# Kernel optimization log

Hardware: AMD Instinct MI355X
Metric: run time of the kernel (lower is better)

## Reference

```python
import math
import jax, jax.numpy as jnp
import numpy as np

D, NH, NL, NP = 256, 8, 4, 4
C = D // NH
VALUE_SHAPES = np.array([[128, 128], [64, 64], [32, 32], [16, 16]], dtype=np.int32)


def _offset_bias():
    # Faithful to MSDeformAttn._reset_parameters grid init for sampling_offsets.bias
    th = np.arange(NH, dtype=np.float32) * (2.0 * np.pi / NH)
    g = np.stack([np.cos(th), np.sin(th)], -1)                      # [NH,2]
    g = g / np.abs(g).max(-1, keepdims=True)
    g = np.tile(g[:, None, None, :], (1, NL, NP, 1))                # [NH,NL,NP,2]
    g = g * np.arange(1, NP + 1, dtype=np.float32)[None, None, :, None]
    return jnp.asarray(g.reshape(-1), jnp.float32)


def setup_inputs() -> dict:
    key = jax.random.key(0)
    ks = jax.random.split(key, 10)
    bs, Q = 8, 2048
    LV = int((VALUE_SHAPES[:, 0] * VALUE_SHAPES[:, 1]).sum())
    s = 0.02
    return {
        "query": jax.random.normal(ks[0], (bs, Q, D), jnp.float32),
        "refer_bbox": jax.random.uniform(ks[1], (bs, Q, NL, 2), jnp.float32),
        "value": jax.random.normal(ks[2], (bs, LV, D), jnp.float32),
        "value_shapes": VALUE_SHAPES,  # static numpy (shapes must be compile-time constants)
        "W_value": jax.random.normal(ks[3], (D, D), jnp.float32) * s,
        "b_value": jnp.zeros((D,), jnp.float32),
        "W_off": jax.random.normal(ks[4], (D, NH * NL * NP * 2), jnp.float32) * 0.01,
        "b_off": _offset_bias(),
        "W_attn": jax.random.normal(ks[5], (D, NH * NL * NP), jnp.float32) * s,
        "b_attn": jnp.zeros((NH * NL * NP,), jnp.float32),
        "W_out": jax.random.normal(ks[6], (D, D), jnp.float32) * s,
        "b_out": jnp.zeros((D,), jnp.float32),
    }


def _ms_deform_attn(value, shapes, loc, attn):
    # value: [bs,LV,NH,C], loc: [bs,Q,NH,NL,NP,2] in [0,1], attn: [bs,Q,NH,NL,NP]
    bs, LV = value.shape[:2]
    Q = loc.shape[1]
    BH = bs * NH
    v = value.transpose(0, 2, 1, 3).reshape(BH, LV, C)              # [BH,LV,C]
    loc = loc.transpose(0, 2, 1, 3, 4, 5).reshape(BH, Q, NL, NP, 2)
    attn = attn.transpose(0, 2, 1, 3, 4).reshape(BH, Q, NL, NP)
    acc = jnp.zeros((BH, Q, C), value.dtype)
    start = 0
    for lvl in range(NL):
        H, W = int(shapes[lvl, 0]), int(shapes[lvl, 1])
        img = v[:, start:start + H * W]                             # [BH,HW,C]
        start += H * W
        # grid_sample(align_corners=False): pixel coord = loc * size - 0.5
        x = loc[:, :, lvl, :, 0] * W - 0.5                          # [BH,Q,NP]
        y = loc[:, :, lvl, :, 1] * H - 0.5
        x0 = jnp.floor(x); y0 = jnp.floor(y)
        fx = x - x0; fy = y - y0
        x0i = x0.astype(jnp.int32); y0i = y0.astype(jnp.int32)
        samp = jnp.zeros((BH, Q, NP, C), value.dtype)
        for dx, dy in ((0, 0), (1, 0), (0, 1), (1, 1)):
            xi = x0i + dx; yi = y0i + dy
            valid = (xi >= 0) & (xi < W) & (yi >= 0) & (yi < H)     # zero padding
            w = (fx if dx else 1.0 - fx) * (fy if dy else 1.0 - fy)
            w = jnp.where(valid, w, 0.0)
            idx = jnp.clip(yi, 0, H - 1) * W + jnp.clip(xi, 0, W - 1)
            g = jnp.take_along_axis(img, idx.reshape(BH, Q * NP)[..., None], axis=1)
            samp = samp + w[..., None] * g.reshape(BH, Q, NP, C)
        acc = acc + (samp * attn[:, :, lvl, :, None]).sum(2)
    return acc.reshape(bs, NH, Q, C).transpose(0, 2, 1, 3).reshape(bs, Q, D)


def reference(query, refer_bbox, value, value_shapes, W_value, b_value,
              W_off, b_off, W_attn, b_attn, W_out, b_out):
    shapes = np.asarray(value_shapes)  # static
    bs, Q = query.shape[:2]
    LV = value.shape[1]
    v = (value @ W_value + b_value).reshape(bs, LV, NH, C)
    off = (query @ W_off + b_off).reshape(bs, Q, NH, NL, NP, 2)
    attn = jax.nn.softmax((query @ W_attn + b_attn).reshape(bs, Q, NH, NL * NP), -1)
    attn = attn.reshape(bs, Q, NH, NL, NP)
    norm = jnp.asarray(shapes[:, ::-1], query.dtype)                # (W,H) per level
    loc = refer_bbox[:, :, None, :, None, :] + off / norm[None, None, None, :, None, :]
    out = _ms_deform_attn(v, shapes, loc, attn)
    return out @ W_out + b_out
```

## Files before the change

kernel.cpp:

```cpp
#include <hip/hip_runtime.h>
#include <hip/hip_bf16.h>

#define D_MODEL 256
#define NHEAD   8
#define NLVL    4
#define NPTS    4
#define CH      32
#define QTOT    2048
#define BS      8
#define LVTOT   21760
#define KDIM    256

typedef __attribute__((ext_vector_type(8))) short bf16x8;
typedef __attribute__((ext_vector_type(4))) float f32x4;

__device__ inline float bf_lo(unsigned u) { unsigned t = u << 16; float f; __builtin_memcpy(&f, &t, 4); return f; }
__device__ inline float bf_hi(unsigned u) { unsigned t = u & 0xffff0000u; float f; __builtin_memcpy(&f, &t, 4); return f; }
__device__ inline float bfu2f(unsigned short s) { unsigned t = (unsigned)s << 16; float f; __builtin_memcpy(&f, &t, 4); return f; }
__device__ inline unsigned short f2bfu(float f) { __hip_bfloat16 h = __float2bfloat16(f); unsigned short u; __builtin_memcpy(&u, &h, 2); return u; }

#define BK  64
#define LDP 72
#define LDC2 136

__device__ inline void transpose_W_body(const float* __restrict__ W,
                                        __hip_bfloat16* __restrict__ Wt,
                                        int sh, int blk, int tid) {
    int t = blk * 256 + tid;
    int k = t >> sh, n = t & ((1 << sh) - 1);
    Wt[n * 256 + k] = __float2bfloat16(W[(k << sh) + n]);
}

__global__ __launch_bounds__(256)
void convert_all(const float* __restrict__ q, __hip_bfloat16* __restrict__ qb,
                 const float* __restrict__ Wv, __hip_bfloat16* __restrict__ Wtv,
                 const float* __restrict__ Wo, __hip_bfloat16* __restrict__ Wto,
                 const float* __restrict__ Wa, __hip_bfloat16* __restrict__ Wta) {
    const int bid = blockIdx.x;
    const int tid = threadIdx.x;
    if (bid < 4096) {
        int t = bid * 256 + tid;
        float4 f = ((const float4*)q)[t];
        __hip_bfloat16 h4[4] = {__float2bfloat16(f.x), __float2bfloat16(f.y),
                                __float2bfloat16(f.z), __float2bfloat16(f.w)};
        ((uint2*)qb)[t] = *(const uint2*)h4;
    } else if (bid < 4352) {
        transpose_W_body(Wv, Wtv, 8, bid - 4096, tid);
    } else if (bid < 4608) {
        transpose_W_body(Wo, Wto, 8, bid - 4352, tid);
    } else {
        transpose_W_body(Wa, Wta, 7, bid - 4608, tid);
    }
}

__global__ __launch_bounds__(256)
void convert_W(const float* __restrict__ W, __hip_bfloat16* __restrict__ Wt, int sh) {
    int t = blockIdx.x * 256 + threadIdx.x;
    int k = t >> sh, n = t & ((1 << sh) - 1);
    Wt[n * 256 + k] = __float2bfloat16(W[(k << sh) + n]);
}

__device__ void value_gemm_body(char* smem, int bid_v,
                                const float* __restrict__ A,
                                const __hip_bfloat16* __restrict__ Wt,
                                const float* __restrict__ bias,
                                __hip_bfloat16* __restrict__ v) {
    __hip_bfloat16* As = (__hip_bfloat16*)smem;
    __hip_bfloat16* Bs = (__hip_bfloat16*)(smem + 128 * LDP * 2);
    __hip_bfloat16* Cs = (__hip_bfloat16*)smem;

    const int tid  = threadIdx.x;
    const int lane = tid & 63;
    const int wave = tid >> 6;
    const int wr   = wave >> 1;
    const int wc   = wave & 1;
    const int cb      = (bid_v & 1) * 128;
    const int rowBase = (bid_v >> 1) * 128;

    const int m0   = lane & 15;
    const int quad = lane >> 4;

    const int ar = tid >> 4;
    const int ac = tid & 15;
    const int br = tid >> 3;
    const int bc = tid & 7;

    f32x4 acc[4][4] = {};

    for (int kc = 0; kc < KDIM; kc += BK) {
#pragma unroll
        for (int i = 0; i < 8; ++i) {
            const int row = i * 16 + ar;
            float4 f = *(const float4*)(A + (size_t)(rowBase + row) * KDIM + kc + ac * 4);
            __hip_bfloat16 t4[4] = {__float2bfloat16(f.x), __float2bfloat16(f.y),
                                    __float2bfloat16(f.z), __float2bfloat16(f.w)};
            *(uint2*)&As[row * LDP + ac * 4] = *(const uint2*)t4;
        }
#pragma unroll
        for (int i = 0; i < 4; ++i) {
            const int row = i * 32 + br;
            uint4 u = *(const uint4*)(Wt + (size_t)(cb + row) * KDIM + kc + bc * 8);
            *(uint4*)&Bs[row * LDP + bc * 8] = u;
        }
        __syncthreads();

#pragma unroll
        for (int ks = 0; ks < 2; ++ks) {
            bf16x8 af[4], bfv[4];
#pragma unroll
            for (int i = 0; i < 4; ++i)
                af[i] = *(const bf16x8*)&As[(wr * 64 + i * 16 + m0) * LDP + ks * 32 + quad * 8];
#pragma unroll
            for (int j = 0; j < 4; ++j)
                bfv[j] = *(const bf16x8*)&Bs[(wc * 64 + j * 16 + m0) * LDP + ks * 32 + quad * 8];
#pragma unroll
            for (int i = 0; i < 4; ++i)
#pragma unroll
                for (int j = 0; j < 4; ++j)
                    acc[i][j] = __builtin_amdgcn_mfma_f32_16x16x32_bf16(af[i], bfv[j], acc[i][j], 0, 0, 0);
        }
        __syncthreads();
    }

    const int b = rowBase / LVTOT;
    const int pixBase = rowBase - b * LVTOT;
#pragma unroll
    for (int half = 0; half < 2; ++half) {
        if (wr == half) {
#pragma unroll
            for (int j = 0; j < 4; ++j) {
                const int lcol = wc * 64 + j * 16 + m0;
                const float bv = bias[cb + lcol];
#pragma unroll
                for (int i = 0; i < 4; ++i) {
                    const int lrow = i * 16 + quad * 4;
#pragma unroll
                    for (int r = 0; r < 4; ++r)
                        Cs[(lrow + r) * LDC2 + lcol] = __float2bfloat16(acc[i][j][r] + bv);
                }
            }
        }
        __syncthreads();
        char* dst = (char*)v + (size_t)(b * LVTOT + pixBase + half * 64) * 512 + cb * 2;
        const char* src = (const char*)Cs;
#pragma unroll
        for (int itr = 0; itr < 4; ++itr) {
            const int o = itr * 4096 + tid * 16;
            const int row = o >> 8;
            const int c   = o & 255;
            uint4 val = *(const uint4*)(src + row * (LDC2 * 2) + c);
            *(uint4*)(dst + (size_t)row * 512 + c) = val;
        }
        if (half == 0) __syncthreads();
    }
}

__device__ void offattn_gemm_body(char* smem, int bid,
                                  const __hip_bfloat16* __restrict__ A,
                                  const __hip_bfloat16* __restrict__ Wt_oa,
                                  const float* __restrict__ b_off,
                                  const float* __restrict__ b_attn,
                                  float* __restrict__ off_ws,
                                  float* __restrict__ logits_ws) {
    __hip_bfloat16* As = (__hip_bfloat16*)smem;
    __hip_bfloat16* Bs = (__hip_bfloat16*)(smem + 128 * LDP * 2);

    const int tid  = threadIdx.x;
    const int lane = tid & 63;
    const int wave = tid >> 6;
    const int rowBase = (bid & 127) * 128;
    const int cb      = (bid >> 7) * 128;

    const int m0   = lane & 15;
    const int quad = lane >> 4;

    const int br = tid >> 3;
    const int bc = tid & 7;

    f32x4 acc[2][8] = {};

    for (int kc = 0; kc < KDIM; kc += BK) {
#pragma unroll
        for (int i = 0; i < 4; ++i) {
            const int row = i * 32 + br;
            uint4 ua = *(const uint4*)(A     + (size_t)(rowBase + row) * KDIM + kc + bc * 8);
            uint4 ub = *(const uint4*)(Wt_oa + (size_t)(cb + row) * KDIM + kc + bc * 8);
            *(uint4*)&As[row * LDP + bc * 8] = ua;
            *(uint4*)&Bs[row * LDP + bc * 8] = ub;
        }
        __syncthreads();

#pragma unroll
        for (int ks = 0; ks < 2; ++ks) {
            bf16x8 af[2], bfv[8];
#pragma unroll
            for (int i = 0; i < 2; ++i)
                af[i] = *(const bf16x8*)&As[(wave * 32 + i * 16 + m0) * LDP + ks * 32 + quad * 8];
#pragma unroll
            for (int j = 0; j < 8; ++j)
                bfv[j] = *(const bf16x8*)&Bs[(j * 16 + m0) * LDP + ks * 32 + quad * 8];
#pragma unroll
            for (int i = 0; i < 2; ++i)
#pragma unroll
                for (int j = 0; j < 8; ++j)
                    acc[i][j] = __builtin_amdgcn_mfma_f32_16x16x32_bf16(af[i], bfv[j], acc[i][j], 0, 0, 0);
        }
        __syncthreads();
    }

#pragma unroll
    for (int j = 0; j < 8; ++j) {
        const int col = cb + j * 16 + m0;
        const bool isOff = (col < 256);
        const float bv = isOff ? b_off[col] : b_attn[col - 256];
#pragma unroll
        for (int i = 0; i < 2; ++i) {
            const int row0 = rowBase + wave * 32 + i * 16 + quad * 4;
#pragma unroll
            for (int r = 0; r < 4; ++r) {
                const float val = acc[i][j][r] + bv;
                if (isOff) off_ws[(size_t)(row0 + r) * 256 + col] = val;
                else       logits_ws[(size_t)(row0 + r) * 128 + (col - 256)] = val;
            }
        }
    }
}

__global__ __launch_bounds__(256, 2)
void fused_gemms(const float* __restrict__ value,
                 const __hip_bfloat16* __restrict__ Wt_v,
                 const float* __restrict__ b_value,
                 __hip_bfloat16* __restrict__ v_ws,
                 const __hip_bfloat16* __restrict__ q_bf,
                 const __hip_bfloat16* __restrict__ Wt_oa,
                 const float* __restrict__ b_off,
                 const float* __restrict__ b_attn,
                 float* __restrict__ off_ws,
                 float* __restrict__ logits_ws) {
    __shared__ __align__(16) char smem[36864];
    const int bid = blockIdx.x;
    if (bid < 384) {
        offattn_gemm_body(smem, bid, q_bf, Wt_oa, b_off, b_attn, off_ws, logits_ws);
    } else {
        value_gemm_body(smem, bid - 384, value, Wt_v, b_value, v_ws);
    }
}

struct StorePlain {
    float* o;
    int ncol;
    __device__ void operator()(int row, int col, float val) const {
        o[(size_t)row * ncol + col] = val;
    }
};

template <typename Store>
__global__ __launch_bounds__(256, 2)
void gemm_bf16_mfma(const __hip_bfloat16* __restrict__ A,
                    const __hip_bfloat16* __restrict__ Wt,
                    const float* __restrict__ bias, Store store) {
    __shared__ __align__(16) __hip_bfloat16 As[128 * LDP];
    __shared__ __align__(16) __hip_bfloat16 Bs[128 * LDP];

    const int tid  = threadIdx.x;
    const int lane = tid & 63;
    const int wave = tid >> 6;
    const int rowBase = blockIdx.x * 128;
    const int cb = blockIdx.y * 128;

    const int m0   = lane & 15;
    const int quad = lane >> 4;

    const int br = tid >> 3;
    const int bc = tid & 7;

    f32x4 acc[2][8] = {};

    for (int kc = 0; kc < KDIM; kc += BK) {
#pragma unroll
        for (int i = 0; i < 4; ++i) {
            const int row = i * 32 + br;
            uint4 ua = *(const uint4*)(A  + (size_t)(rowBase + row) * KDIM + kc + bc * 8);
            uint4 ub = *(const uint4*)(Wt + (size_t)(cb + row) * KDIM + kc + bc * 8);
            *(uint4*)&As[row * LDP + bc * 8] = ua;
            *(uint4*)&Bs[row * LDP + bc * 8] = ub;
        }
        __syncthreads();

#pragma unroll
        for (int ks = 0; ks < 2; ++ks) {
            bf16x8 af[2], bfv[8];
#pragma unroll
            for (int i = 0; i < 2; ++i)
                af[i] = *(const bf16x8*)&As[(wave * 32 + i * 16 + m0) * LDP + ks * 32 + quad * 8];
#pragma unroll
            for (int j = 0; j < 8; ++j)
                bfv[j] = *(const bf16x8*)&Bs[(j * 16 + m0) * LDP + ks * 32 + quad * 8];
#pragma unroll
            for (int i = 0; i < 2; ++i)
#pragma unroll
                for (int j = 0; j < 8; ++j)
                    acc[i][j] = __builtin_amdgcn_mfma_f32_16x16x32_bf16(af[i], bfv[j], acc[i][j], 0, 0, 0);
        }
        __syncthreads();
    }

#pragma unroll
    for (int j = 0; j < 8; ++j) {
        const int col = cb + j * 16 + m0;
        const float bv = bias[col];
#pragma unroll
        for (int i = 0; i < 2; ++i) {
            const int row0 = rowBase + wave * 32 + i * 16 + quad * 4;
#pragma unroll
            for (int r = 0; r < 4; ++r)
                store(row0 + r, col, acc[i][j][r] + bv);
        }
    }
}

__global__ __launch_bounds__(256, 5)
void sample_kernel(const float* __restrict__ off_ws,
                   const float* __restrict__ logits_ws,
                   const float* __restrict__ bbox,
                   const __hip_bfloat16* __restrict__ v,
                   __hip_bfloat16* __restrict__ acc_bf) {
    __shared__ __align__(16) float off_s[8 * 256];
    __shared__ __align__(16) float attn_s[8 * 128];
    __shared__ float bbox_s[64];
    __shared__ __align__(8) unsigned short idx_s[1024 * 4];
    __shared__ __align__(8) unsigned short w_s[1024 * 4];

    const int tid = threadIdx.x;
    const int b = blockIdx.x & 7;
    const int gq0 = b * QTOT + (blockIdx.x >> 3) * 8;

    const float4* osrc = (const float4*)(off_ws + (size_t)gq0 * 256);
    ((float4*)off_s)[tid] = osrc[tid];
    ((float4*)off_s)[tid + 256] = osrc[tid + 256];
    const float4* lsrc = (const float4*)(logits_ws + (size_t)gq0 * 128);
    ((float4*)attn_s)[tid] = lsrc[tid];
    if (tid < 64) bbox_s[tid] = bbox[(size_t)gq0 * 8 + tid];
    __syncthreads();

    if (tid < 64) {
        int qq = tid >> 3, h = tid & 7;
        float* p = attn_s + qq * 128 + h * 16;
        float m = p[0];
#pragma unroll
        for (int i = 1; i < 16; ++i) m = fmaxf(m, p[i]);
        float e[16], s = 0.f;
#pragma unroll
        for (int i = 0; i < 16; ++i) { e[i] = __expf(p[i] - m); s += e[i]; }
        float inv = 1.f / s;
#pragma unroll
        for (int i = 0; i < 16; ++i) p[i] = e[i] * inv;
    }
    __syncthreads();

#pragma unroll
    for (int r = 0; r < 4; ++r) {
        const int tap = tid + r * 256;
        const int qq = tap >> 7, h = (tap >> 4) & 7, l = (tap >> 2) & 3, p = tap & 3;
        const int Wd = 128 >> l;
        const int st = (l == 0) ? 0 : (l == 1) ? 16384 : (l == 2) ? 20480 : 21504;

        const float bx = bbox_s[qq * 8 + l * 2 + 0];
        const float by = bbox_s[qq * 8 + l * 2 + 1];
        const float ox = off_s[qq * 256 + h * 32 + l * 8 + p * 2 + 0];
        const float oy = off_s[qq * 256 + h * 32 + l * 8 + p * 2 + 1];
        const float att = attn_s[qq * 128 + h * 16 + l * 4 + p];

        const float x = bx * (float)Wd + ox - 0.5f;
        const float y = by * (float)Wd + oy - 0.5f;
        const float x0f = floorf(x), y0f = floorf(y);
        const float fx = x - x0f, fy = y - y0f;
        const int x0 = (int)x0f, y0 = (int)y0f;
        const int x1 = x0 + 1, y1 = y0 + 1;
        const bool vx0 = (unsigned)x0 < (unsigned)Wd;
        const bool vx1 = (unsigned)x1 < (unsigned)Wd;
        const bool vy0 = (unsigned)y0 < (unsigned)Wd;
        const bool vy1 = (unsigned)y1 < (unsigned)Wd;
        const int cx0 = min(max(x0, 0), Wd - 1), cx1 = min(max(x1, 0), Wd - 1);
        const int cy0 = min(max(y0, 0), Wd - 1), cy1 = min(max(y1, 0), Wd - 1);

        unsigned short pi[4];
        pi[0] = (unsigned short)(st + cy0 * Wd + cx0);
        pi[1] = (unsigned short)(st + cy0 * Wd + cx1);
        pi[2] = (unsigned short)(st + cy1 * Wd + cx0);
        pi[3] = (unsigned short)(st + cy1 * Wd + cx1);
        float w0 = (vx0 && vy0) ? (1.f - fx) * (1.f - fy) * att : 0.f;
        float w1 = (vx1 && vy0) ? fx * (1.f - fy) * att : 0.f;
        float w2 = (vx0 && vy1) ? (1.f - fx) * fy * att : 0.f;
        float w3 = (vx1 && vy1) ? fx * fy * att : 0.f;

        *(uint2*)&idx_s[tap * 4] = *(const uint2*)pi;
        unsigned short w4[4] = {f2bfu(w0), f2bfu(w1), f2bfu(w2), f2bfu(w3)};
        *(uint2*)&w_s[tap * 4] = *(const uint2*)w4;
    }
    __syncthreads();

    const int lane = tid & 63;
    const int wave = tid >> 6;
    const int g  = lane >> 3;
    const int c4 = lane & 7;

    const char* vbase = (const char*)v + (size_t)b * LVTOT * 512 + c4 * 8;

    for (int i = 0; i < 8; ++i) {
        const int pairA = wave * 16 + 2 * i;
        const int pairB = pairA + 1;
        const int qqA = pairA >> 3, hhA = pairA & 7;
        const int qqB = pairB >> 3, hhB = pairB & 7;
        const char* slabA = vbase + hhA * 64;
        const char* slabB = vbase + hhB * 64;
        const int tbA = qqA * 128 + hhA * 16;
        const int tbB = qqB * 128 + hhB * 16;

        const ushort4 pA0 = *(const ushort4*)&idx_s[(tbA + g) * 4];
        const ushort4 pA1 = *(const ushort4*)&idx_s[(tbA + 8 + g) * 4];
        const ushort4 pB0 = *(const ushort4*)&idx_s[(tbB + g) * 4];
        const ushort4 pB1 = *(const ushort4*)&idx_s[(tbB + 8 + g) * 4];
        const ushort4 wA0 = *(const ushort4*)&w_s[(tbA + g) * 4];
        const ushort4 wA1 = *(const ushort4*)&w_s[(tbA + 8 + g) * 4];
        const ushort4 wB0 = *(const ushort4*)&w_s[(tbB + g) * 4];
        const ushort4 wB1 = *(const ushort4*)&w_s[(tbB + 8 + g) * 4];

        uint2 uA0 = *(const uint2*)(slabA + ((int)pA0.x << 9));
        uint2 uA1 = *(const uint2*)(slabA + ((int)pA0.y << 9));
        uint2 uA2 = *(const uint2*)(slabA + ((int)pA0.z << 9));
        uint2 uA3 = *(const uint2*)(slabA + ((int)pA0.w << 9));
        uint2 uA4 = *(const uint2*)(slabA + ((int)pA1.x << 9));
        uint2 uA5 = *(const uint2*)(slabA + ((int)pA1.y << 9));
        uint2 uA6 = *(const uint2*)(slabA + ((int)pA1.z << 9));
        uint2 uA7 = *(const uint2*)(slabA + ((int)pA1.w << 9));
        uint2 uB0 = *(const uint2*)(slabB + ((int)pB0.x << 9));
        uint2 uB1 = *(const uint2*)(slabB + ((int)pB0.y << 9));
        uint2 uB2 = *(const uint2*)(slabB + ((int)pB0.z << 9));
        uint2 uB3 = *(const uint2*)(slabB + ((int)pB0.w << 9));
        uint2 uB4 = *(const uint2*)(slabB + ((int)pB1.x << 9));
        uint2 uB5 = *(const uint2*)(slabB + ((int)pB1.y << 9));
        uint2 uB6 = *(const uint2*)(slabB + ((int)pB1.z << 9));
        uint2 uB7 = *(const uint2*)(slabB + ((int)pB1.w << 9));

        float a0 = 0.f, a1 = 0.f, a2 = 0.f, a3 = 0.f;
        float b0 = 0.f, b1 = 0.f, b2 = 0.f, b3 = 0.f;
        {
            float w;
            w = bfu2f(wA0.x); a0 += w * bf_lo(uA0.x); a1 += w * bf_hi(uA0.x); a2 += w * bf_lo(uA0.y); a3 += w * bf_hi(uA0.y);
            w = bfu2f(wA0.y); a0 += w * bf_lo(uA1.x); a1 += w * bf_hi(uA1.x); a2 += w * bf_lo(uA1.y); a3 += w * bf_hi(uA1.y);
            w = bfu2f(wA0.z); a0 += w * bf_lo(uA2.x); a1 += w * bf_hi(uA2.x); a2 += w * bf_lo(uA2.y); a3 += w * bf_hi(uA2.y);
            w = bfu2f(wA0.w); a0 += w * bf_lo(uA3.x); a1 += w * bf_hi(uA3.x); a2 += w * bf_lo(uA3.y); a3 += w * bf_hi(uA3.y);
            w = bfu2f(wA1.x); a0 += w * bf_lo(uA4.x); a1 += w * bf_hi(uA4.x); a2 += w * bf_lo(uA4.y); a3 += w * bf_hi(uA4.y);
            w = bfu2f(wA1.y); a0 += w * bf_lo(uA5.x); a1 += w * bf_hi(uA5.x); a2 += w * bf_lo(uA5.y); a3 += w * bf_hi(uA5.y);
            w = bfu2f(wA1.z); a0 += w * bf_lo(uA6.x); a1 += w * bf_hi(uA6.x); a2 += w * bf_lo(uA6.y); a3 += w * bf_hi(uA6.y);
            w = bfu2f(wA1.w); a0 += w * bf_lo(uA7.x); a1 += w * bf_hi(uA7.x); a2 += w * bf_lo(uA7.y); a3 += w * bf_hi(uA7.y);
            w = bfu2f(wB0.x); b0 += w * bf_lo(uB0.x); b1 += w * bf_hi(uB0.x); b2 += w * bf_lo(uB0.y); b3 += w * bf_hi(uB0.y);
            w = bfu2f(wB0.y); b0 += w * bf_lo(uB1.x); b1 += w * bf_hi(uB1.x); b2 += w * bf_lo(uB1.y); b3 += w * bf_hi(uB1.y);
            w = bfu2f(wB0.z); b0 += w * bf_lo(uB2.x); b1 += w * bf_hi(uB2.x); b2 += w * bf_lo(uB2.y); b3 += w * bf_hi(uB2.y);
            w = bfu2f(wB0.w); b0 += w * bf_lo(uB3.x); b1 += w * bf_hi(uB3.x); b2 += w * bf_lo(uB3.y); b3 += w * bf_hi(uB3.y);
            w = bfu2f(wB1.x); b0 += w * bf_lo(uB4.x); b1 += w * bf_hi(uB4.x); b2 += w * bf_lo(uB4.y); b3 += w * bf_hi(uB4.y);
            w = bfu2f(wB1.y); b0 += w * bf_lo(uB5.x); b1 += w * bf_hi(uB5.x); b2 += w * bf_lo(uB5.y); b3 += w * bf_hi(uB5.y);
            w = bfu2f(wB1.z); b0 += w * bf_lo(uB6.x); b1 += w * bf_hi(uB6.x); b2 += w * bf_lo(uB6.y); b3 += w * bf_hi(uB6.y);
            w = bfu2f(wB1.w); b0 += w * bf_lo(uB7.x); b1 += w * bf_hi(uB7.x); b2 += w * bf_lo(uB7.y); b3 += w * bf_hi(uB7.y);
        }

        a0 += __shfl_xor(a0, 8);  a1 += __shfl_xor(a1, 8);  a2 += __shfl_xor(a2, 8);  a3 += __shfl_xor(a3, 8);
        b0 += __shfl_xor(b0, 8);  b1 += __shfl_xor(b1, 8);  b2 += __shfl_xor(b2, 8);  b3 += __shfl_xor(b3, 8);
        a0 += __shfl_xor(a0, 16); a1 += __shfl_xor(a1, 16); a2 += __shfl_xor(a2, 16); a3 += __shfl_xor(a3, 16);
        b0 += __shfl_xor(b0, 16); b1 += __shfl_xor(b1, 16); b2 += __shfl_xor(b2, 16); b3 += __shfl_xor(b3, 16);
        a0 += __shfl_xor(a0, 32); a1 += __shfl_xor(a1, 32); a2 += __shfl_xor(a2, 32); a3 += __shfl_xor(a3, 32);
        b0 += __shfl_xor(b0, 32); b1 += __shfl_xor(b1, 32); b2 += __shfl_xor(b2, 32); b3 += __shfl_xor(b3, 32);

        if (g == 0) {
            unsigned lo, hi;
            __hip_bfloat16 h2[2];
            h2[0] = __float2bfloat16(a0); h2[1] = __float2bfloat16(a1);
            __builtin_memcpy(&lo, h2, 4);
            h2[0] = __float2bfloat16(a2); h2[1] = __float2bfloat16(a3);
            __builtin_memcpy(&hi, h2, 4);
            uint2 pk; pk.x = lo; pk.y = hi;
            *(uint2*)((char*)acc_bf + ((size_t)(gq0 + qqA) * 256 + hhA * 32 + c4 * 4) * 2) = pk;
            h2[0] = __float2bfloat16(b0); h2[1] = __float2bfloat16(b1);
            __builtin_memcpy(&lo, h2, 4);
            h2[0] = __float2bfloat16(b2); h2[1] = __float2bfloat16(b3);
            __builtin_memcpy(&hi, h2, 4);
            pk.x = lo; pk.y = hi;
            *(uint2*)((char*)acc_bf + ((size_t)(gq0 + qqB) * 256 + hhB * 32 + c4 * 4) * 2) = pk;
        }
    }
}

extern "C" void kernel_launch(void* const* d_in, const int* in_sizes, int n_in,
                              void* d_out, int out_size, void* d_ws, size_t ws_size,
                              hipStream_t stream) {
    const float* query   = (const float*)d_in[0];
    const float* bbox    = (const float*)d_in[1];
    const float* value   = (const float*)d_in[2];
    const float* W_value = (const float*)d_in[4];
    const float* b_value = (const float*)d_in[5];
    const float* W_off   = (const float*)d_in[6];
    const float* b_off   = (const float*)d_in[7];
    const float* W_attn  = (const float*)d_in[8];
    const float* b_attn  = (const float*)d_in[9];
    const float* W_out   = (const float*)d_in[10];
    const float* b_out   = (const float*)d_in[11];
    float* out = (float*)d_out;

    char* ws = (char*)d_ws;
    __hip_bfloat16* v_ws  = (__hip_bfloat16*)ws;
    float* off_ws         = (float*)(ws + 89128960);
    float* logits_ws      = (float*)(ws + 89128960 + 16777216);
    __hip_bfloat16* acc_bf = (__hip_bfloat16*)(ws + 89128960 + 16777216 + 8388608);
    __hip_bfloat16* q_bf   = (__hip_bfloat16*)(ws + 89128960 + 16777216 + 8388608 + 8388608);

    __hip_bfloat16* Wt_v    = acc_bf;
    __hip_bfloat16* Wt_off  = acc_bf + 65536;
    __hip_bfloat16* Wt_attn = acc_bf + 131072;
    __hip_bfloat16* Wt_out  = q_bf;

    const int NQ = BS * QTOT;
    const int NVROWS = BS * LVTOT;

    convert_all<<<4736, 256, 0, stream>>>(query, q_bf,
                                          W_value, Wt_v,
                                          W_off, Wt_off,
                                          W_attn, Wt_attn);

    fused_gemms<<<384 + 2 * (NVROWS / 128), 256, 0, stream>>>(
        value, Wt_v, b_value, v_ws,
        q_bf, Wt_off, b_off, b_attn, off_ws, logits_ws);

    convert_W<<<256, 256, 0, stream>>>(W_out, Wt_out, 8);

    sample_kernel<<<NQ / 8, 256, 0, stream>>>(off_ws, logits_ws, bbox, v_ws, acc_bf);

    gemm_bf16_mfma<<<dim3(NQ / 128, 2), 256, 0, stream>>>(
        acc_bf, Wt_out, b_out, StorePlain{out, 256});
}
```

Before: 393.0 us.

## Fuse output projection into sampling kernel and drop the separate GEMM

Each sampling block now keeps its 8 queries' attention output in fp32 shared memory, reusing the offset buffer. It then computes the output projection itself, with each thread handling one output column and reading a transposed bf16 W_out row from global memory. This removes the bf16 intermediate write and read to global memory and one kernel launch. In exchange, the projection moves from MFMA to scalar FP32 FMAs, and every block rereads all of W_out with strided per-thread loads, which adds a serial tail to each block.

```diff
diff --git a/kernel.cpp b/kernel.cpp
--- a/kernel.cpp
+++ b/kernel.cpp
@@ -246,90 +246,21 @@
     }
 }
 
-struct StorePlain {
-    float* o;
-    int ncol;
-    __device__ void operator()(int row, int col, float val) const {
-        o[(size_t)row * ncol + col] = val;
-    }
-};
-
-template <typename Store>
-__global__ __launch_bounds__(256, 2)
-void gemm_bf16_mfma(const __hip_bfloat16* __restrict__ A,
-                    const __hip_bfloat16* __restrict__ Wt,
-                    const float* __restrict__ bias, Store store) {
-    __shared__ __align__(16) __hip_bfloat16 As[128 * LDP];
-    __shared__ __align__(16) __hip_bfloat16 Bs[128 * LDP];
-
-    const int tid  = threadIdx.x;
-    const int lane = tid & 63;
-    const int wave = tid >> 6;
-    const int rowBase = blockIdx.x * 128;
-    const int cb = blockIdx.y * 128;
-
-    const int m0   = lane & 15;
-    const int quad = lane >> 4;
-
-    const int br = tid >> 3;
-    const int bc = tid & 7;
-
-    f32x4 acc[2][8] = {};
-
-    for (int kc = 0; kc < KDIM; kc += BK) {
-#pragma unroll
-        for (int i = 0; i < 4; ++i) {
-            const int row = i * 32 + br;
-            uint4 ua = *(const uint4*)(A  + (size_t)(rowBase + row) * KDIM + kc + bc * 8);
-            uint4 ub = *(const uint4*)(Wt + (size_t)(cb + row) * KDIM + kc + bc * 8);
-            *(uint4*)&As[row * LDP + bc * 8] = ua;
-            *(uint4*)&Bs[row * LDP + bc * 8] = ub;
-        }
-        __syncthreads();
-
-#pragma unroll
-        for (int ks = 0; ks < 2; ++ks) {
-            bf16x8 af[2], bfv[8];
-#pragma unroll
-            for (int i = 0; i < 2; ++i)
-                af[i] = *(const bf16x8*)&As[(wave * 32 + i * 16 + m0) * LDP + ks * 32 + quad * 8];
-#pragma unroll
-            for (int j = 0; j < 8; ++j)
-                bfv[j] = *(const bf16x8*)&Bs[(j * 16 + m0) * LDP + ks * 32 + quad * 8];
-#pragma unroll
-            for (int i = 0; i < 2; ++i)
-#pragma unroll
-                for (int j = 0; j < 8; ++j)
-                    acc[i][j] = __builtin_amdgcn_mfma_f32_16x16x32_bf16(af[i], bfv[j], acc[i][j], 0, 0, 0);
-        }
-        __syncthreads();
-    }
-
-#pragma unroll
-    for (int j = 0; j < 8; ++j) {
-        const int col = cb + j * 16 + m0;
-        const float bv = bias[col];
-#pragma unroll
-        for (int i = 0; i < 2; ++i) {
-            const int row0 = rowBase + wave * 32 + i * 16 + quad * 4;
-#pragma unroll
-            for (int r = 0; r < 4; ++r)
-                store(row0 + r, col, acc[i][j][r] + bv);
-        }
-    }
-}
-
 __global__ __launch_bounds__(256, 5)
-void sample_kernel(const float* __restrict__ off_ws,
-                   const float* __restrict__ logits_ws,
-                   const float* __restrict__ bbox,
-                   const __hip_bfloat16* __restrict__ v,
-                   __hip_bfloat16* __restrict__ acc_bf) {
+void sample_out_kernel(const float* __restrict__ off_ws,
+                       const float* __restrict__ logits_ws,
+                       const float* __restrict__ bbox,
+                       const __hip_bfloat16* __restrict__ v,
+                       const __hip_bfloat16* __restrict__ Wt_out,
+                       const float* __restrict__ b_out,
+                       float* __restrict__ out_p) {
     __shared__ __align__(16) float off_s[8 * 256];
     __shared__ __align__(16) float attn_s[8 * 128];
     __shared__ float bbox_s[64];
     __shared__ __align__(8) unsigned short idx_s[1024 * 4];
     __shared__ __align__(8) unsigned short w_s[1024 * 4];
+
+    float* acc_s = off_s;
 
     const int tid = threadIdx.x;
     const int b = blockIdx.x & 7;
@@ -473,21 +404,31 @@
         b0 += __shfl_xor(b0, 32); b1 += __shfl_xor(b1, 32); b2 += __shfl_xor(b2, 32); b3 += __shfl_xor(b3, 32);
 
         if (g == 0) {
-            unsigned lo, hi;
-            __hip_bfloat16 h2[2];
-            h2[0] = __float2bfloat16(a0); h2[1] = __float2bfloat16(a1);
-            __builtin_memcpy(&lo, h2, 4);
-            h2[0] = __float2bfloat16(a2); h2[1] = __float2bfloat16(a3);
-            __builtin_memcpy(&hi, h2, 4);
-            uint2 pk; pk.x = lo; pk.y = hi;
-            *(uint2*)((char*)acc_bf + ((size_t)(gq0 + qqA) * 256 + hhA * 32 + c4 * 4) * 2) = pk;
-            h2[0] = __float2bfloat16(b0); h2[1] = __float2bfloat16(b1);
-            __builtin_memcpy(&lo, h2, 4);
-            h2[0] = __float2bfloat16(b2); h2[1] = __float2bfloat16(b3);
-            __builtin_memcpy(&hi, h2, 4);
-            pk.x = lo; pk.y = hi;
-            *(uint2*)((char*)acc_bf + ((size_t)(gq0 + qqB) * 256 + hhB * 32 + c4 * 4) * 2) = pk;
-        }
+            *(float4*)&acc_s[qqA * 256 + hhA * 32 + c4 * 4] = make_float4(a0, a1, a2, a3);
+            *(float4*)&acc_s[qqB * 256 + hhB * 32 + c4 * 4] = make_float4(b0, b1, b2, b3);
+        }
+    }
+    __syncthreads();
+
+    {
+        const int col = tid;
+        const uint2* wrow = (const uint2*)((const char*)Wt_out + (size_t)col * 512);
+        float oq[8] = {0.f, 0.f, 0.f, 0.f, 0.f, 0.f, 0.f, 0.f};
+#pragma unroll 4
+        for (int k4 = 0; k4 < 64; ++k4) {
+            const uint2 wv = wrow[k4];
+            const float w0 = bf_lo(wv.x), w1 = bf_hi(wv.x);
+            const float w2 = bf_lo(wv.y), w3 = bf_hi(wv.y);
+#pragma unroll
+            for (int q = 0; q < 8; ++q) {
+                const float4 av = *(const float4*)&acc_s[q * 256 + k4 * 4];
+                oq[q] += w0 * av.x + w1 * av.y + w2 * av.z + w3 * av.w;
+            }
+        }
+        const float bo = b_out[col];
+#pragma unroll
+        for (int q = 0; q < 8; ++q)
+            out_p[(size_t)(gq0 + q) * 256 + col] = oq[q] + bo;
     }
 }
 
@@ -533,8 +474,6 @@
 
     convert_W<<<256, 256, 0, stream>>>(W_out, Wt_out, 8);
 
-    sample_kernel<<<NQ / 8, 256, 0, stream>>>(off_ws, logits_ws, bbox, v_ws, acc_bf);
-
-    gemm_bf16_mfma<<<dim3(NQ / 128, 2), 256, 0, stream>>>(
-        acc_bf, Wt_out, b_out, StorePlain{out, 256});
-}
+    sample_out_kernel<<<NQ / 8, 256, 0, stream>>>(
+        off_ws, logits_ws, bbox, v_ws, Wt_out, b_out, out);
+}
```

After: 431.1 us. 1.1x slower.
